# Kernel optimization log

Measured on AMD Instinct MI355X. Metric: run time of the kernel, lower is better.

## Reference

```python
import jax, jax.numpy as jnp
import numpy as np

N, M = 1024, 32
FN, FE = 64, 32
AGG_N, AGG_E = 128, 64
OUT_N, OUT_E = 64, 32


def _build_indices(n, m):
    nip, eip = [], []
    k = 0
    for i in range(1, n):
        j0 = max(0, i - m)
        nip += list(range(j0, i))
        eip += list(range(k, k + i - j0))
        k += i - j0
    n1 = np.array(nip, np.int32)
    eT = np.array(eip, np.int32)
    n2 = np.concatenate([np.full(min(i, m), i, np.int32) for i in range(1, n)])
    # padded previous-node window indices (0 = zero pad slot)
    prev_nodes = np.zeros(n * m, np.int32)
    k = 0
    for i in range(n):
        t = min(i, m)
        prev_nodes[(i + 1) * m - t:(i + 1) * m] = np.arange(k, k + t) + 1
        k += t
    n_e = k
    norm_node = np.full(n, 1.0 / m, np.float32)
    for i in range(1, m):
        norm_node[i] = 1.0 / i
    prev_edges = np.zeros(n_e * m, np.int32)
    k = 0
    e = 0
    for i in range(n):
        j0 = max(0, i - m)
        for j in range(j0, i):
            if j > j0:
                prev_edges[(e + 1) * m - (j - j0):(e + 1) * m] = np.arange(k, k + j - j0) + 1
            e += 1
        k += i - j0
    norm_edge = np.ones(n_e, np.float32)
    k = 0
    for i in range(1, n):
        t = min(i, m)
        for j in range(t):
            if j > 0:
                norm_edge[k] = 1.0 / j
            k += 1
    return n1, eT, n2, prev_nodes, norm_node, prev_edges, norm_edge, n_e

N1, ET, N2, PREV_N, NORM_N, PREV_E, NORM_E, NE = _build_indices(N, M)
N1 = jnp.asarray(N1); ET = jnp.asarray(ET); N2 = jnp.asarray(N2)
PREV_N = jnp.asarray(PREV_N); PREV_E = jnp.asarray(PREV_E)
NORM_N = jnp.asarray(NORM_N); NORM_E = jnp.asarray(NORM_E)


def setup_inputs() -> dict:
    key = jax.random.key(0)
    ks = jax.random.split(key, 20)
    s = 0.02
    inp = {
        'input_nodes': jax.random.normal(ks[0], (2, N, FN), jnp.float32),
        'input_edges': jax.random.normal(ks[1], (2, NE, FE), jnp.float32),
        # node-branch MLPs (exclude_last=False)
        'Wan1': jax.random.normal(ks[2], (2 * FN + FE, 2 * AGG_N)) * s,
        'ban1': jnp.zeros((2 * AGG_N,)),
        'Wan2': jax.random.normal(ks[3], (2 * AGG_N, AGG_N)) * s,
        'ban2': jnp.zeros((AGG_N,)),
        'Wln1': jax.random.normal(ks[4], (AGG_N + FN, AGG_N + FN)) * s,
        'bln1': jnp.zeros((AGG_N + FN,)),
        'Wln2': jax.random.normal(ks[5], (AGG_N + FN, OUT_N)) * s,
        'bln2': jnp.zeros((OUT_N,)),
        # edge-branch MLPs
        'Wae1': jax.random.normal(ks[6], (FN + FE, 2 * AGG_E)) * s,
        'bae1': jnp.zeros((2 * AGG_E,)),
        'Wae2': jax.random.normal(ks[7], (2 * AGG_E, AGG_E)) * s,
        'bae2': jnp.zeros((AGG_E,)),
        'Wle1': jax.random.normal(ks[8], (AGG_E + FE, AGG_E + FE)) * s,
        'ble1': jnp.zeros((AGG_E + FE,)),
        'Wle2': jax.random.normal(ks[9], (AGG_E + FE, OUT_E)) * s,
        'ble2': jnp.zeros((OUT_E,)),
    }
    return inp


def _mlp2(x, W1, b1, W2, b2):
    return jax.nn.relu(jax.nn.relu(x @ W1 + b1) @ W2 + b2)


def reference(input_nodes, input_edges, Wan1, ban1, Wan2, ban2, Wln1, bln1, Wln2, bln2,
              Wae1, bae1, Wae2, bae2, Wle1, ble1, Wle2, ble2):
    B = input_nodes.shape[0]
    # gather node-edge pairs [B, NE, FN+FE] and node-edge-node triples [B, NE, 2FN+FE]
    pairs = jnp.concatenate([input_nodes[:, N1], input_edges[:, ET]], axis=-1)
    triples = jnp.concatenate([input_nodes[:, N1], input_edges[:, ET], input_nodes[:, N2]], axis=-1)
    # node branch (exclude_last=False -> triples)
    hn = _mlp2(triples, Wan1, ban1, Wan2, ban2)                     # [B, NE, AGG_N]
    hn = jnp.concatenate([jnp.zeros((B, 1, AGG_N), hn.dtype), hn], axis=1)
    pn = hn[:, PREV_N].reshape(B, N, M, AGG_N).sum(axis=2)          # padded window sum
    pn = pn * NORM_N[None, :, None]
    nodes_in = jnp.concatenate([pn, input_nodes], axis=-1)
    out_nodes = _mlp2(nodes_in, Wln1, bln1, Wln2, bln2)             # activation_nodes = relu
    # edge branch (pairs)
    he = _mlp2(pairs, Wae1, bae1, Wae2, bae2)                       # [B, NE, AGG_E]
    he = jnp.concatenate([jnp.zeros((B, 1, AGG_E), he.dtype), he], axis=1)
    pe = he[:, PREV_E].reshape(B, NE, M, AGG_E).sum(axis=2)
    pe = pe * NORM_E[None, :, None]
    edges_in = jnp.concatenate([pe, input_edges], axis=-1)
    out_edges = _mlp2(edges_in, Wle1, ble1, Wle2, ble2)             # activation_edges = relu
    return out_nodes, out_edges
```

## Files before the change

### kernel.cpp

```cpp
#include <hip/hip_runtime.h>
#include <cstdint>

#define NN    1024
#define MM    32
#define NEDGE 32240
#define MROWS 64480

typedef unsigned short ushort_t;

typedef __bf16 bf16x8 __attribute__((ext_vector_type(8)));
typedef float  floatx4 __attribute__((ext_vector_type(4)));

__device__ __forceinline__ float b2f(ushort_t u) {
    union { unsigned int i; float f; } v; v.i = ((unsigned int)u) << 16; return v.f;
}
__device__ __forceinline__ ushort_t f2b(float f) {
    unsigned int u = __builtin_bit_cast(unsigned int, f);
    u = (u + 0x7FFFu + ((u >> 16) & 1u)) >> 16;
    return (ushort_t)u;
}
__device__ __forceinline__ int edge_base(int i) {
    return (i <= MM) ? ((i * (i - 1)) >> 1) : (496 + (i - MM) * MM);
}
__device__ __forceinline__ void edge_ij(int e, int& i, int& j) {
    if (e < 496) {
        i = (int)((1.0f + sqrtf(8.0f * (float)e + 1.0f)) * 0.5f);
        while (((i * (i - 1)) >> 1) > e) --i;
        while (((i * (i + 1)) >> 1) <= e) ++i;
        j = e - ((i * (i - 1)) >> 1);
    } else {
        int q = e - 496;
        i = MM + (q >> 5);
        j = i - MM + (q & 31);
    }
}

__global__ __launch_bounds__(256) void k_pack(
        const float* an1, const float* an2, const float* ae1, const float* ae2,
        const float* le1, const float* le2, const float* ln1, const float* ln2,
        const float* nodes, const float* edges,
        ushort_t* pan1, ushort_t* pan2, ushort_t* pae1, ushort_t* pae2,
        ushort_t* ple1, ushort_t* ple2, ushort_t* pln1, ushort_t* pln2,
        ushort_t* nodesb, ushort_t* ein, int2* ijt) {
    __shared__ float tile[32][33];
    const int bid = blockIdx.x;
    const int tid = threadIdx.x;
    if (bid < 152) {
        const float* s; ushort_t* d; int K, N, t;
        if (bid < 40)       { s = an1; d = pan1; K = 160; N = 256; t = bid;       }
        else if (bid < 72)  { s = an2; d = pan2; K = 256; N = 128; t = bid - 40;  }
        else if (bid < 84)  { s = ae1; d = pae1; K = 96;  N = 128; t = bid - 72;  }
        else if (bid < 92)  { s = ae2; d = pae2; K = 128; N = 64;  t = bid - 84;  }
        else if (bid < 101) { s = le1; d = ple1; K = 96;  N = 96;  t = bid - 92;  }
        else if (bid < 104) { s = le2; d = ple2; K = 96;  N = 32;  t = bid - 101; }
        else if (bid < 140) { s = ln1; d = pln1; K = 192; N = 192; t = bid - 104; }
        else                { s = ln2; d = pln2; K = 192; N = 64;  t = bid - 140; }
        int ntn = N >> 5;
        int tk = t / ntn, tn = t - tk * ntn;
        int k0 = tk * 32, n0 = tn * 32;
        int tx = tid & 31, ty = tid >> 5;
#pragma unroll
        for (int m = 0; m < 4; ++m)
            tile[ty + m * 8][tx] = s[(size_t)(k0 + ty + m * 8) * N + n0 + tx];
        __syncthreads();
#pragma unroll
        for (int m = 0; m < 4; ++m)
            d[(size_t)(n0 + ty + m * 8) * K + k0 + tx] = f2b(tile[tx][ty + m * 8]);
    } else if (bid < 280) {
        int i4 = (bid - 152) * 256 + tid;
        float4 v = ((const float4*)nodes)[i4];
        uint2 o;
        o.x = (unsigned)f2b(v.x) | ((unsigned)f2b(v.y) << 16);
        o.y = (unsigned)f2b(v.z) | ((unsigned)f2b(v.w) << 16);
        ((uint2*)nodesb)[i4] = o;
    } else if (bid < 2295) {
        int idx = (bid - 280) * 256 + tid;
        int r = idx >> 3, c4 = idx & 7;
        float4 v = ((const float4*)(edges + (size_t)r * 32))[c4];
        uint2 o;
        o.x = (unsigned)f2b(v.x) | ((unsigned)f2b(v.y) << 16);
        o.y = (unsigned)f2b(v.z) | ((unsigned)f2b(v.w) << 16);
        *(uint2*)(ein + (size_t)r * 96 + 64 + c4 * 4) = o;
    } else {
        int e = (bid - 2295) * 256 + tid;
        if (e < NEDGE) { int i, j; edge_ij(e, i, j); ijt[e] = make_int2(i, j); }
    }
}

__global__ __launch_bounds__(256, 2) void k_agg(
        const ushort_t* __restrict__ nodesb, const float* __restrict__ edges,
        const int2* __restrict__ ijt,
        const ushort_t* __restrict__ pan1, const float* __restrict__ ban1,
        const ushort_t* __restrict__ pan2, const float* __restrict__ ban2,
        const ushort_t* __restrict__ pae1, const float* __restrict__ bae1,
        const ushort_t* __restrict__ pae2, const float* __restrict__ bae2,
        ushort_t* __restrict__ hn, ushort_t* __restrict__ he) {
    __shared__ alignas(16) ushort_t L1[32 * 168];
    __shared__ alignas(16) ushort_t L2[32 * 264];
    const int tid = threadIdx.x;
    const int w = tid >> 6, l = tid & 63, lrow = l & 15, lq = l >> 4;
    floatx4 zero = {0.f, 0.f, 0.f, 0.f};

    if (blockIdx.x < 2015) {
        const int mt = blockIdx.x;
        int2 ij[8];
#pragma unroll
        for (int k = 0; k < 8; ++k) {
            int r = mt * 32 + w * 8 + k;
            int e = (r >= NEDGE) ? r - NEDGE : r;
            ij[k] = ijt[e];
        }
#pragma unroll
        for (int k = 0; k < 8; ++k) {
            int rr = w * 8 + k;
            int r = mt * 32 + rr;
            int b = (r >= NEDGE) ? 1 : 0;
            ushort_t* xr = L1 + rr * 168;
            const unsigned* nj = (const unsigned*)(nodesb + (size_t)(b * NN + ij[k].y) * 64);
            const unsigned* ni = (const unsigned*)(nodesb + (size_t)(b * NN + ij[k].x) * 64);
            if (l < 32) { ((unsigned*)xr)[l] = nj[l]; ((unsigned*)xr)[48 + l] = ni[l]; }
            else        xr[64 + (l - 32)] = f2b(edges[(size_t)r * 32 + (l - 32)]);
        }
        {
            bf16x8 b1[5][4]; float v1[4];
#pragma unroll
            for (int kt = 0; kt < 5; ++kt)
#pragma unroll
                for (int nt = 0; nt < 4; ++nt)
                    b1[kt][nt] = *(const bf16x8*)(pan1 + (size_t)(w * 64 + nt * 16 + lrow) * 160 + kt * 32 + lq * 8);
#pragma unroll
            for (int nt = 0; nt < 4; ++nt) v1[nt] = ban1[w * 64 + nt * 16 + lrow];
            __syncthreads();
            floatx4 acc[2][4];
#pragma unroll
            for (int s = 0; s < 2; ++s)
#pragma unroll
                for (int nt = 0; nt < 4; ++nt) acc[s][nt] = zero;
#pragma unroll
            for (int s = 0; s < 2; ++s)
#pragma unroll
                for (int kt = 0; kt < 5; ++kt) {
                    bf16x8 a = *(const bf16x8*)&L1[(s * 16 + lrow) * 168 + kt * 32 + lq * 8];
#pragma unroll
                    for (int nt = 0; nt < 4; ++nt)
                        acc[s][nt] = __builtin_amdgcn_mfma_f32_16x16x32_bf16(a, b1[kt][nt], acc[s][nt], 0, 0, 0);
                }
#pragma unroll
            for (int s = 0; s < 2; ++s)
#pragma unroll
                for (int nt = 0; nt < 4; ++nt) {
                    int col = w * 64 + nt * 16 + lrow;
#pragma unroll
                    for (int r_ = 0; r_ < 4; ++r_)
                        L2[(s * 16 + lq * 4 + r_) * 264 + col] = f2b(fmaxf(acc[s][nt][r_] + v1[nt], 0.f));
                }
        }
        __syncthreads();
        {
            bf16x8 b2[8][2]; float v2[2];
#pragma unroll
            for (int kt = 0; kt < 8; ++kt)
#pragma unroll
                for (int nt = 0; nt < 2; ++nt)
                    b2[kt][nt] = *(const bf16x8*)(pan2 + (size_t)(w * 32 + nt * 16 + lrow) * 256 + kt * 32 + lq * 8);
#pragma unroll
            for (int nt = 0; nt < 2; ++nt) v2[nt] = ban2[w * 32 + nt * 16 + lrow];
            floatx4 a2[2][2];
#pragma unroll
            for (int s = 0; s < 2; ++s) { a2[s][0] = zero; a2[s][1] = zero; }
#pragma unroll
            for (int s = 0; s < 2; ++s)
#pragma unroll
                for (int kt = 0; kt < 8; ++kt) {
                    bf16x8 a = *(const bf16x8*)&L2[(s * 16 + lrow) * 264 + kt * 32 + lq * 8];
#pragma unroll
                    for (int nt = 0; nt < 2; ++nt)
                        a2[s][nt] = __builtin_amdgcn_mfma_f32_16x16x32_bf16(a, b2[kt][nt], a2[s][nt], 0, 0, 0);
                }
#pragma unroll
            for (int s = 0; s < 2; ++s)
#pragma unroll
                for (int nt = 0; nt < 2; ++nt) {
                    int col = w * 32 + nt * 16 + lrow;
#pragma unroll
                    for (int r_ = 0; r_ < 4; ++r_)
                        hn[(size_t)(mt * 32 + s * 16 + lq * 4 + r_) * 128 + col] = f2b(fmaxf(a2[s][nt][r_] + v2[nt], 0.f));
                }
        }
    } else {
        const int mt = blockIdx.x - 2015;
        int jj[8];
#pragma unroll
        for (int k = 0; k < 8; ++k) {
            int r = mt * 32 + w * 8 + k;
            int e = (r >= NEDGE) ? r - NEDGE : r;
            jj[k] = ijt[e].y;
        }
#pragma unroll
        for (int k = 0; k < 8; ++k) {
            int rr = w * 8 + k;
            int r = mt * 32 + rr;
            int b = (r >= NEDGE) ? 1 : 0;
            ushort_t* xr = L1 + rr * 104;
            const unsigned* nj = (const unsigned*)(nodesb + (size_t)(b * NN + jj[k]) * 64);
            if (l < 32) ((unsigned*)xr)[l] = nj[l];
            else        xr[64 + (l - 32)] = f2b(edges[(size_t)r * 32 + (l - 32)]);
        }
        {
            bf16x8 e1[3][2]; float v1[2];
#pragma unroll
            for (int kt = 0; kt < 3; ++kt)
#pragma unroll
                for (int nt = 0; nt < 2; ++nt)
                    e1[kt][nt] = *(const bf16x8*)(pae1 + (size_t)(w * 32 + nt * 16 + lrow) * 96 + kt * 32 + lq * 8);
#pragma unroll
            for (int nt = 0; nt < 2; ++nt) v1[nt] = bae1[w * 32 + nt * 16 + lrow];
            __syncthreads();
            floatx4 acc[2][2];
#pragma unroll
            for (int s = 0; s < 2; ++s) { acc[s][0] = zero; acc[s][1] = zero; }
#pragma unroll
            for (int s = 0; s < 2; ++s)
#pragma unroll
                for (int kt = 0; kt < 3; ++kt) {
                    bf16x8 a = *(const bf16x8*)&L1[(s * 16 + lrow) * 104 + kt * 32 + lq * 8];
#pragma unroll
                    for (int nt = 0; nt < 2; ++nt)
                        acc[s][nt] = __builtin_amdgcn_mfma_f32_16x16x32_bf16(a, e1[kt][nt], acc[s][nt], 0, 0, 0);
                }
#pragma unroll
            for (int s = 0; s < 2; ++s)
#pragma unroll
                for (int nt = 0; nt < 2; ++nt) {
                    int col = w * 32 + nt * 16 + lrow;
#pragma unroll
                    for (int r_ = 0; r_ < 4; ++r_)
                        L2[(s * 16 + lq * 4 + r_) * 136 + col] = f2b(fmaxf(acc[s][nt][r_] + v1[nt], 0.f));
                }
        }
        __syncthreads();
        {
            bf16x8 e2[4];
#pragma unroll
            for (int kt = 0; kt < 4; ++kt)
                e2[kt] = *(const bf16x8*)(pae2 + (size_t)(w * 16 + lrow) * 128 + kt * 32 + lq * 8);
            float v2 = bae2[w * 16 + lrow];
            floatx4 a2[2] = {zero, zero};
#pragma unroll
            for (int s = 0; s < 2; ++s)
#pragma unroll
                for (int kt = 0; kt < 4; ++kt) {
                    bf16x8 a = *(const bf16x8*)&L2[(s * 16 + lrow) * 136 + kt * 32 + lq * 8];
                    a2[s] = __builtin_amdgcn_mfma_f32_16x16x32_bf16(a, e2[kt], a2[s], 0, 0, 0);
                }
#pragma unroll
            for (int s = 0; s < 2; ++s) {
                int col = w * 16 + lrow;
#pragma unroll
                for (int r_ = 0; r_ < 4; ++r_)
                    he[(size_t)(mt * 32 + s * 16 + lq * 4 + r_) * 64 + col] = f2b(fmaxf(a2[s][r_] + v2, 0.f));
            }
        }
    }
}

__global__ __launch_bounds__(256) void k_mid(
        const ushort_t* __restrict__ hn, const ushort_t* __restrict__ he,
        ushort_t* __restrict__ pn, ushort_t* __restrict__ ein) {
    const int tid = threadIdx.x;
    if (blockIdx.x < 512) {
        int ri = blockIdx.x * 4 + (tid >> 6);
        int l = tid & 63;
        int b = ri >> 10, i = ri & 1023;
        int t = min(i, MM);
        int base = b * NEDGE + edge_base(i);
        const unsigned* hp = (const unsigned*)(hn + (size_t)base * 128) + l;
        float a0 = 0.f, a1 = 0.f, c0 = 0.f, c1 = 0.f;
        int p = 0;
        for (; p + 1 < t; p += 2) {
            unsigned u = hp[(size_t)p * 64];
            unsigned v = hp[(size_t)(p + 1) * 64];
            a0 += b2f((ushort_t)(u & 0xffff)); a1 += b2f((ushort_t)(u >> 16));
            c0 += b2f((ushort_t)(v & 0xffff)); c1 += b2f((ushort_t)(v >> 16));
        }
        if (p < t) {
            unsigned u = hp[(size_t)p * 64];
            a0 += b2f((ushort_t)(u & 0xffff)); a1 += b2f((ushort_t)(u >> 16));
        }
        float inv = 1.0f / (float)max(t, 1);
        unsigned o = (unsigned)f2b((a0 + c0) * inv) | ((unsigned)f2b((a1 + c1) * inv) << 16);
        ((unsigned*)(pn + (size_t)ri * 128))[l] = o;
    } else {
        int bi = blockIdx.x - 512;
        int b = bi >> 10, i = bi & 1023;
        int t = min(i, MM);
        if (t == 0) return;
        int base = b * NEDGE + edge_base(i);
        __shared__ alignas(16) ushort_t hw[32 * 64];
        for (int u = tid; u < t * 8; u += 256)
            ((uint4*)hw)[u] = ((const uint4*)he)[(size_t)base * 8 + u];
        __syncthreads();
        if (tid < 64) {
            float run = 0.f;
            for (int p = 0; p < t; ++p) {
                float v = (p == 0) ? 0.f : run / (float)p;
                ein[(size_t)(base + p) * 96 + tid] = f2b(v);
                run += b2f(hw[p * 64 + tid]);
            }
        }
    }
}

__global__ __launch_bounds__(192) void k_final(
        const ushort_t* __restrict__ pn, const ushort_t* __restrict__ nodesb,
        const ushort_t* __restrict__ pln1, const float* __restrict__ bln1,
        const ushort_t* __restrict__ pln2, const float* __restrict__ bln2,
        float* __restrict__ out_nodes,
        const ushort_t* __restrict__ ein, const ushort_t* __restrict__ ple1,
        const float* __restrict__ ble1, const ushort_t* __restrict__ ple2,
        const float* __restrict__ ble2, float* __restrict__ out_edges) {
    __shared__ alignas(16) ushort_t LA[32 * 200];
    __shared__ alignas(16) ushort_t LB[32 * 200];
    const int tid = threadIdx.x;
    const int w = tid >> 6, l = tid & 63, lrow = l & 15, lq = l >> 4;
    floatx4 zero = {0.f, 0.f, 0.f, 0.f};

    if (blockIdx.x < 64) {
        int tile = blockIdx.x;
        for (int u = tid; u < 768; u += 192) {
            int row = u / 24, c = u - row * 24;
            int ri = tile * 32 + row;
            int b = ri >> 10, i = ri & 1023;
            const uint4* src = (c < 16) ? ((const uint4*)(pn + (size_t)ri * 128) + c)
                                        : ((const uint4*)(nodesb + (size_t)(b * NN + i) * 64) + (c - 16));
            *(uint4*)&LA[row * 200 + c * 8] = *src;
        }
        bf16x8 f1[6][4]; float v1[4];
#pragma unroll
        for (int kt = 0; kt < 6; ++kt)
#pragma unroll
            for (int nt = 0; nt < 4; ++nt)
                f1[kt][nt] = *(const bf16x8*)(pln1 + (size_t)(w * 64 + nt * 16 + lrow) * 192 + kt * 32 + lq * 8);
#pragma unroll
        for (int nt = 0; nt < 4; ++nt) v1[nt] = bln1[w * 64 + nt * 16 + lrow];
        __syncthreads();

        floatx4 acc[2][4];
#pragma unroll
        for (int s = 0; s < 2; ++s)
#pragma unroll
            for (int nt = 0; nt < 4; ++nt) acc[s][nt] = zero;
#pragma unroll
        for (int s = 0; s < 2; ++s)
#pragma unroll
            for (int kt = 0; kt < 6; ++kt) {
                bf16x8 a = *(const bf16x8*)&LA[(s * 16 + lrow) * 200 + kt * 32 + lq * 8];
#pragma unroll
                for (int nt = 0; nt < 4; ++nt)
                    acc[s][nt] = __builtin_amdgcn_mfma_f32_16x16x32_bf16(a, f1[kt][nt], acc[s][nt], 0, 0, 0);
            }
#pragma unroll
        for (int s = 0; s < 2; ++s)
#pragma unroll
            for (int nt = 0; nt < 4; ++nt) {
                int col = w * 64 + nt * 16 + lrow;
#pragma unroll
                for (int r_ = 0; r_ < 4; ++r_)
                    LB[(s * 16 + lq * 4 + r_) * 200 + col] = f2b(fmaxf(acc[s][nt][r_] + v1[nt], 0.f));
            }
        __syncthreads();

        if (w < 2) {
            bf16x8 f2[6][2]; float v2[2];
#pragma unroll
            for (int kt = 0; kt < 6; ++kt)
#pragma unroll
                for (int nt = 0; nt < 2; ++nt)
                    f2[kt][nt] = *(const bf16x8*)(pln2 + (size_t)(w * 32 + nt * 16 + lrow) * 192 + kt * 32 + lq * 8);
#pragma unroll
            for (int nt = 0; nt < 2; ++nt) v2[nt] = bln2[w * 32 + nt * 16 + lrow];
            floatx4 a2[2][2];
#pragma unroll
            for (int s = 0; s < 2; ++s) { a2[s][0] = zero; a2[s][1] = zero; }
#pragma unroll
            for (int s = 0; s < 2; ++s)
#pragma unroll
                for (int kt = 0; kt < 6; ++kt) {
                    bf16x8 a = *(const bf16x8*)&LB[(s * 16 + lrow) * 200 + kt * 32 + lq * 8];
#pragma unroll
                    for (int nt = 0; nt < 2; ++nt)
                        a2[s][nt] = __builtin_amdgcn_mfma_f32_16x16x32_bf16(a, f2[kt][nt], a2[s][nt], 0, 0, 0);
                }
#pragma unroll
            for (int s = 0; s < 2; ++s)
#pragma unroll
                for (int nt = 0; nt < 2; ++nt) {
                    int col = w * 32 + nt * 16 + lrow;
#pragma unroll
                    for (int r_ = 0; r_ < 4; ++r_)
                        out_nodes[(size_t)(tile * 32 + s * 16 + lq * 4 + r_) * 64 + col] =
                            fmaxf(a2[s][nt][r_] + v2[nt], 0.f);
                }
        }
    } else {
        int mt = blockIdx.x - 64;
        for (int k = 0; k < 11; ++k) {
            int rr = w * 11 + k;
            if (rr >= 32) break;
            unsigned* xrow = (unsigned*)(LA + rr * 104);
            const unsigned* src = (const unsigned*)(ein + (size_t)(mt * 32 + rr) * 96);
            if (l < 48) xrow[l] = src[l];
        }
        bf16x8 fb1[3][2]; float v1[2];
#pragma unroll
        for (int kt = 0; kt < 3; ++kt)
#pragma unroll
            for (int nt = 0; nt < 2; ++nt)
                fb1[kt][nt] = *(const bf16x8*)(ple1 + (size_t)(w * 32 + nt * 16 + lrow) * 96 + kt * 32 + lq * 8);
#pragma unroll
        for (int nt = 0; nt < 2; ++nt) v1[nt] = ble1[w * 32 + nt * 16 + lrow];
        bf16x8 fb2[3]; float v2 = 0.f;
        if (w < 2) {
#pragma unroll
            for (int kt = 0; kt < 3; ++kt)
                fb2[kt] = *(const bf16x8*)(ple2 + (size_t)(w * 16 + lrow) * 96 + kt * 32 + lq * 8);
            v2 = ble2[w * 16 + lrow];
        }
        __syncthreads();

        floatx4 acc[2][2];
#pragma unroll
        for (int s = 0; s < 2; ++s) { acc[s][0] = zero; acc[s][1] = zero; }
#pragma unroll
        for (int s = 0; s < 2; ++s)
#pragma unroll
            for (int kt = 0; kt < 3; ++kt) {
                bf16x8 a = *(const bf16x8*)&LA[(s * 16 + lrow) * 104 + kt * 32 + lq * 8];
#pragma unroll
                for (int nt = 0; nt < 2; ++nt)
                    acc[s][nt] = __builtin_amdgcn_mfma_f32_16x16x32_bf16(a, fb1[kt][nt], acc[s][nt], 0, 0, 0);
            }
#pragma unroll
        for (int s = 0; s < 2; ++s)
#pragma unroll
            for (int nt = 0; nt < 2; ++nt) {
                int col = w * 32 + nt * 16 + lrow;
#pragma unroll
                for (int r_ = 0; r_ < 4; ++r_)
                    LB[(s * 16 + lq * 4 + r_) * 104 + col] = f2b(fmaxf(acc[s][nt][r_] + v1[nt], 0.f));
            }
        __syncthreads();

        if (w < 2) {
            floatx4 a2[2] = {zero, zero};
#pragma unroll
            for (int s = 0; s < 2; ++s)
#pragma unroll
                for (int kt = 0; kt < 3; ++kt) {
                    bf16x8 a = *(const bf16x8*)&LB[(s * 16 + lrow) * 104 + kt * 32 + lq * 8];
                    a2[s] = __builtin_amdgcn_mfma_f32_16x16x32_bf16(a, fb2[kt], a2[s], 0, 0, 0);
                }
#pragma unroll
            for (int s = 0; s < 2; ++s) {
                int col = w * 16 + lrow;
#pragma unroll
                for (int r_ = 0; r_ < 4; ++r_)
                    out_edges[(size_t)(mt * 32 + s * 16 + lq * 4 + r_) * 32 + col] = fmaxf(a2[s][r_] + v2, 0.f);
            }
        }
    }
}

extern "C" void kernel_launch(void* const* d_in, const int* in_sizes, int n_in,
                              void* d_out, int out_size, void* d_ws, size_t ws_size,
                              hipStream_t stream) {
    const float* nodes = (const float*)d_in[0];
    const float* edges = (const float*)d_in[1];
    const float* Wan1 = (const float*)d_in[2];  const float* ban1 = (const float*)d_in[3];
    const float* Wan2 = (const float*)d_in[4];  const float* ban2 = (const float*)d_in[5];
    const float* Wln1 = (const float*)d_in[6];  const float* bln1 = (const float*)d_in[7];
    const float* Wln2 = (const float*)d_in[8];  const float* bln2 = (const float*)d_in[9];
    const float* Wae1 = (const float*)d_in[10]; const float* bae1 = (const float*)d_in[11];
    const float* Wae2 = (const float*)d_in[12]; const float* bae2 = (const float*)d_in[13];
    const float* Wle1 = (const float*)d_in[14]; const float* ble1 = (const float*)d_in[15];
    const float* Wle2 = (const float*)d_in[16]; const float* ble2 = (const float*)d_in[17];

    char* ws = (char*)d_ws;
    size_t o = 0;
    auto alloc = [&](size_t bytes) -> void* {
        void* r = ws + o;
        o += (bytes + 255) & ~(size_t)255;
        return r;
    };
    ushort_t* hn     = (ushort_t*)alloc((size_t)MROWS * 128 * 2);
    ushort_t* he     = (ushort_t*)alloc((size_t)MROWS * 64 * 2);
    ushort_t* ein    = (ushort_t*)alloc((size_t)MROWS * 96 * 2);
    ushort_t* pn     = (ushort_t*)alloc((size_t)2048 * 128 * 2);
    ushort_t* nodesb = (ushort_t*)alloc((size_t)2 * NN * 64 * 2);
    int2*     ijt    = (int2*)alloc((size_t)NEDGE * 8);
    ushort_t* pan1 = (ushort_t*)alloc(160 * 256 * 2);
    ushort_t* pan2 = (ushort_t*)alloc(256 * 128 * 2);
    ushort_t* pae1 = (ushort_t*)alloc(96 * 128 * 2);
    ushort_t* pae2 = (ushort_t*)alloc(128 * 64 * 2);
    ushort_t* ple1 = (ushort_t*)alloc(96 * 96 * 2);
    ushort_t* ple2 = (ushort_t*)alloc(96 * 32 * 2);
    ushort_t* pln1 = (ushort_t*)alloc(192 * 192 * 2);
    ushort_t* pln2 = (ushort_t*)alloc(192 * 64 * 2);

    float* out_nodes = (float*)d_out;
    float* out_edges = (float*)d_out + 2 * NN * 64;

    k_pack<<<2421, 256, 0, stream>>>(Wan1, Wan2, Wae1, Wae2, Wle1, Wle2, Wln1, Wln2,
                                     nodes, edges,
                                     pan1, pan2, pae1, pae2, ple1, ple2, pln1, pln2,
                                     nodesb, ein, ijt);
    k_agg<<<4030, 256, 0, stream>>>(nodesb, edges, ijt,
                                    pan1, ban1, pan2, ban2,
                                    pae1, bae1, pae2, bae2, hn, he);
    k_mid<<<2560, 256, 0, stream>>>(hn, he, pn, ein);
    k_final<<<64 + 2015, 192, 0, stream>>>(pn, nodesb, pln1, bln1, pln2, bln2, out_nodes,
                                           ein, ple1, ble1, ple2, ble2, out_edges);

    (void)in_sizes; (void)n_in; (void)out_size; (void)ws_size;
}
```

Baseline: 167.5 us.

## Load MFMA A-operands directly to registers, widen k_agg blocks, split node-window sum

k_agg and k_final now gather each wave's MFMA A fragments straight from global memory into registers instead of staging them in LDS, which removes one LDS round trip and one barrier per tile. k_agg goes from 256 to 512 threads so each wave computes fewer output columns. Its second-layer B-fragment loads are moved before the remaining barrier. In k_mid the node-window sum now uses one block per node, with four wave groups each summing part of the window and a shared-memory reduction at the end. In exchange, every wave reloads the same A rows, so global and L2 traffic rises, and k_agg's higher launch-bounds target tightens the register budget.

```diff
diff --git a/kernel.cpp b/kernel.cpp
--- a/kernel.cpp
+++ b/kernel.cpp
@@ -18,6 +18,12 @@
     unsigned int u = __builtin_bit_cast(unsigned int, f);
     u = (u + 0x7FFFu + ((u >> 16) & 1u)) >> 16;
     return (ushort_t)u;
+}
+__device__ __forceinline__ bf16x8 cvt8(float4 a, float4 b) {
+    union { bf16x8 v; ushort_t u[8]; } r;
+    r.u[0] = f2b(a.x); r.u[1] = f2b(a.y); r.u[2] = f2b(a.z); r.u[3] = f2b(a.w);
+    r.u[4] = f2b(b.x); r.u[5] = f2b(b.y); r.u[6] = f2b(b.z); r.u[7] = f2b(b.w);
+    return r.v;
 }
 __device__ __forceinline__ int edge_base(int i) {
     return (i <= MM) ? ((i * (i - 1)) >> 1) : (496 + (i - MM) * MM);
@@ -87,7 +93,7 @@
     }
 }
 
-__global__ __launch_bounds__(256, 2) void k_agg(
+__global__ __launch_bounds__(512, 4) void k_agg(
         const ushort_t* __restrict__ nodesb, const float* __restrict__ edges,
         const int2* __restrict__ ijt,
         const ushort_t* __restrict__ pan1, const float* __restrict__ ban1,
@@ -95,162 +101,128 @@
         const ushort_t* __restrict__ pae1, const float* __restrict__ bae1,
         const ushort_t* __restrict__ pae2, const float* __restrict__ bae2,
         ushort_t* __restrict__ hn, ushort_t* __restrict__ he) {
-    __shared__ alignas(16) ushort_t L1[32 * 168];
-    __shared__ alignas(16) ushort_t L2[32 * 264];
+    __shared__ alignas(16) ushort_t LS[32 * 264];
     const int tid = threadIdx.x;
     const int w = tid >> 6, l = tid & 63, lrow = l & 15, lq = l >> 4;
     floatx4 zero = {0.f, 0.f, 0.f, 0.f};
 
     if (blockIdx.x < 2015) {
         const int mt = blockIdx.x;
-        int2 ij[8];
-#pragma unroll
-        for (int k = 0; k < 8; ++k) {
-            int r = mt * 32 + w * 8 + k;
-            int e = (r >= NEDGE) ? r - NEDGE : r;
-            ij[k] = ijt[e];
-        }
-#pragma unroll
-        for (int k = 0; k < 8; ++k) {
-            int rr = w * 8 + k;
-            int r = mt * 32 + rr;
-            int b = (r >= NEDGE) ? 1 : 0;
-            ushort_t* xr = L1 + rr * 168;
-            const unsigned* nj = (const unsigned*)(nodesb + (size_t)(b * NN + ij[k].y) * 64);
-            const unsigned* ni = (const unsigned*)(nodesb + (size_t)(b * NN + ij[k].x) * 64);
-            if (l < 32) { ((unsigned*)xr)[l] = nj[l]; ((unsigned*)xr)[48 + l] = ni[l]; }
-            else        xr[64 + (l - 32)] = f2b(edges[(size_t)r * 32 + (l - 32)]);
-        }
-        {
-            bf16x8 b1[5][4]; float v1[4];
+        bf16x8 A[2][5];
+#pragma unroll
+        for (int s = 0; s < 2; ++s) {
+            int r = mt * 32 + s * 16 + lrow;
+            int off = (r >= NEDGE) ? NEDGE : 0;
+            int2 ij = ijt[r - off];
+            int bN = off ? NN : 0;
+            const ushort_t* nj = nodesb + (size_t)(bN + ij.y) * 64;
+            const ushort_t* ni = nodesb + (size_t)(bN + ij.x) * 64;
+            A[s][0] = *(const bf16x8*)(nj + lq * 8);
+            A[s][1] = *(const bf16x8*)(nj + 32 + lq * 8);
+            const float* er = edges + (size_t)r * 32 + lq * 8;
+            A[s][2] = cvt8(*(const float4*)er, *(const float4*)(er + 4));
+            A[s][3] = *(const bf16x8*)(ni + lq * 8);
+            A[s][4] = *(const bf16x8*)(ni + 32 + lq * 8);
+        }
+        bf16x8 b1[5][2]; float v1[2];
+#pragma unroll
+        for (int kt = 0; kt < 5; ++kt)
+#pragma unroll
+            for (int nt = 0; nt < 2; ++nt)
+                b1[kt][nt] = *(const bf16x8*)(pan1 + (size_t)(w * 32 + nt * 16 + lrow) * 160 + kt * 32 + lq * 8);
+#pragma unroll
+        for (int nt = 0; nt < 2; ++nt) v1[nt] = ban1[w * 32 + nt * 16 + lrow];
+
+        floatx4 acc[2][2];
+#pragma unroll
+        for (int s = 0; s < 2; ++s) { acc[s][0] = zero; acc[s][1] = zero; }
+#pragma unroll
+        for (int s = 0; s < 2; ++s)
 #pragma unroll
             for (int kt = 0; kt < 5; ++kt)
 #pragma unroll
-                for (int nt = 0; nt < 4; ++nt)
-                    b1[kt][nt] = *(const bf16x8*)(pan1 + (size_t)(w * 64 + nt * 16 + lrow) * 160 + kt * 32 + lq * 8);
-#pragma unroll
-            for (int nt = 0; nt < 4; ++nt) v1[nt] = ban1[w * 64 + nt * 16 + lrow];
-            __syncthreads();
-            floatx4 acc[2][4];
-#pragma unroll
-            for (int s = 0; s < 2; ++s)
-#pragma unroll
-                for (int nt = 0; nt < 4; ++nt) acc[s][nt] = zero;
-#pragma unroll
-            for (int s = 0; s < 2; ++s)
-#pragma unroll
-                for (int kt = 0; kt < 5; ++kt) {
-                    bf16x8 a = *(const bf16x8*)&L1[(s * 16 + lrow) * 168 + kt * 32 + lq * 8];
-#pragma unroll
-                    for (int nt = 0; nt < 4; ++nt)
-                        acc[s][nt] = __builtin_amdgcn_mfma_f32_16x16x32_bf16(a, b1[kt][nt], acc[s][nt], 0, 0, 0);
-                }
-#pragma unroll
-            for (int s = 0; s < 2; ++s)
-#pragma unroll
-                for (int nt = 0; nt < 4; ++nt) {
-                    int col = w * 64 + nt * 16 + lrow;
-#pragma unroll
-                    for (int r_ = 0; r_ < 4; ++r_)
-                        L2[(s * 16 + lq * 4 + r_) * 264 + col] = f2b(fmaxf(acc[s][nt][r_] + v1[nt], 0.f));
-                }
-        }
-        __syncthreads();
-        {
-            bf16x8 b2[8][2]; float v2[2];
-#pragma unroll
-            for (int kt = 0; kt < 8; ++kt)
-#pragma unroll
                 for (int nt = 0; nt < 2; ++nt)
-                    b2[kt][nt] = *(const bf16x8*)(pan2 + (size_t)(w * 32 + nt * 16 + lrow) * 256 + kt * 32 + lq * 8);
-#pragma unroll
-            for (int nt = 0; nt < 2; ++nt) v2[nt] = ban2[w * 32 + nt * 16 + lrow];
-            floatx4 a2[2][2];
-#pragma unroll
-            for (int s = 0; s < 2; ++s) { a2[s][0] = zero; a2[s][1] = zero; }
-#pragma unroll
-            for (int s = 0; s < 2; ++s)
-#pragma unroll
-                for (int kt = 0; kt < 8; ++kt) {
-                    bf16x8 a = *(const bf16x8*)&L2[(s * 16 + lrow) * 264 + kt * 32 + lq * 8];
-#pragma unroll
-                    for (int nt = 0; nt < 2; ++nt)
-                        a2[s][nt] = __builtin_amdgcn_mfma_f32_16x16x32_bf16(a, b2[kt][nt], a2[s][nt], 0, 0, 0);
-                }
-#pragma unroll
-            for (int s = 0; s < 2; ++s)
-#pragma unroll
-                for (int nt = 0; nt < 2; ++nt) {
-                    int col = w * 32 + nt * 16 + lrow;
-#pragma unroll
-                    for (int r_ = 0; r_ < 4; ++r_)
-                        hn[(size_t)(mt * 32 + s * 16 + lq * 4 + r_) * 128 + col] = f2b(fmaxf(a2[s][nt][r_] + v2[nt], 0.f));
-                }
+                    acc[s][nt] = __builtin_amdgcn_mfma_f32_16x16x32_bf16(A[s][kt], b1[kt][nt], acc[s][nt], 0, 0, 0);
+#pragma unroll
+        for (int s = 0; s < 2; ++s)
+#pragma unroll
+            for (int nt = 0; nt < 2; ++nt) {
+                int col = w * 32 + nt * 16 + lrow;
+#pragma unroll
+                for (int r_ = 0; r_ < 4; ++r_)
+                    LS[(s * 16 + lq * 4 + r_) * 264 + col] = f2b(fmaxf(acc[s][nt][r_] + v1[nt], 0.f));
+            }
+        bf16x8 b2[8];
+#pragma unroll
+        for (int kt = 0; kt < 8; ++kt)
+            b2[kt] = *(const bf16x8*)(pan2 + (size_t)(w * 16 + lrow) * 256 + kt * 32 + lq * 8);
+        float v2 = ban2[w * 16 + lrow];
+        __syncthreads();
+
+        floatx4 a2[2] = {zero, zero};
+#pragma unroll
+        for (int s = 0; s < 2; ++s)
+#pragma unroll
+            for (int kt = 0; kt < 8; ++kt) {
+                bf16x8 a = *(const bf16x8*)&LS[(s * 16 + lrow) * 264 + kt * 32 + lq * 8];
+                a2[s] = __builtin_amdgcn_mfma_f32_16x16x32_bf16(a, b2[kt], a2[s], 0, 0, 0);
+            }
+#pragma unroll
+        for (int s = 0; s < 2; ++s) {
+            int col = w * 16 + lrow;
+#pragma unroll
+            for (int r_ = 0; r_ < 4; ++r_)
+                hn[(size_t)(mt * 32 + s * 16 + lq * 4 + r_) * 128 + col] = f2b(fmaxf(a2[s][r_] + v2, 0.f));
         }
     } else {
         const int mt = blockIdx.x - 2015;
-        int jj[8];
-#pragma unroll
-        for (int k = 0; k < 8; ++k) {
-            int r = mt * 32 + w * 8 + k;
-            int e = (r >= NEDGE) ? r - NEDGE : r;
-            jj[k] = ijt[e].y;
-        }
-#pragma unroll
-        for (int k = 0; k < 8; ++k) {
-            int rr = w * 8 + k;
-            int r = mt * 32 + rr;
-            int b = (r >= NEDGE) ? 1 : 0;
-            ushort_t* xr = L1 + rr * 104;
-            const unsigned* nj = (const unsigned*)(nodesb + (size_t)(b * NN + jj[k]) * 64);
-            if (l < 32) ((unsigned*)xr)[l] = nj[l];
-            else        xr[64 + (l - 32)] = f2b(edges[(size_t)r * 32 + (l - 32)]);
-        }
-        {
-            bf16x8 e1[3][2]; float v1[2];
+        bf16x8 A[2][3];
+#pragma unroll
+        for (int s = 0; s < 2; ++s) {
+            int r = mt * 32 + s * 16 + lrow;
+            int off = (r >= NEDGE) ? NEDGE : 0;
+            int2 ij = ijt[r - off];
+            int bN = off ? NN : 0;
+            const ushort_t* nj = nodesb + (size_t)(bN + ij.y) * 64;
+            A[s][0] = *(const bf16x8*)(nj + lq * 8);
+            A[s][1] = *(const bf16x8*)(nj + 32 + lq * 8);
+            const float* er = edges + (size_t)r * 32 + lq * 8;
+            A[s][2] = cvt8(*(const float4*)er, *(const float4*)(er + 4));
+        }
+        bf16x8 e1[3];
+#pragma unroll
+        for (int kt = 0; kt < 3; ++kt)
+            e1[kt] = *(const bf16x8*)(pae1 + (size_t)(w * 16 + lrow) * 96 + kt * 32 + lq * 8);
+        float v1 = bae1[w * 16 + lrow];
+
+        floatx4 acc[2] = {zero, zero};
+#pragma unroll
+        for (int s = 0; s < 2; ++s)
 #pragma unroll
             for (int kt = 0; kt < 3; ++kt)
-#pragma unroll
-                for (int nt = 0; nt < 2; ++nt)
-                    e1[kt][nt] = *(const bf16x8*)(pae1 + (size_t)(w * 32 + nt * 16 + lrow) * 96 + kt * 32 + lq * 8);
-#pragma unroll
-            for (int nt = 0; nt < 2; ++nt) v1[nt] = bae1[w * 32 + nt * 16 + lrow];
-            __syncthreads();
-            floatx4 acc[2][2];
-#pragma unroll
-            for (int s = 0; s < 2; ++s) { acc[s][0] = zero; acc[s][1] = zero; }
-#pragma unroll
-            for (int s = 0; s < 2; ++s)
-#pragma unroll
-                for (int kt = 0; kt < 3; ++kt) {
-                    bf16x8 a = *(const bf16x8*)&L1[(s * 16 + lrow) * 104 + kt * 32 + lq * 8];
-#pragma unroll
-                    for (int nt = 0; nt < 2; ++nt)
-                        acc[s][nt] = __builtin_amdgcn_mfma_f32_16x16x32_bf16(a, e1[kt][nt], acc[s][nt], 0, 0, 0);
-                }
-#pragma unroll
-            for (int s = 0; s < 2; ++s)
-#pragma unroll
-                for (int nt = 0; nt < 2; ++nt) {
-                    int col = w * 32 + nt * 16 + lrow;
-#pragma unroll
-                    for (int r_ = 0; r_ < 4; ++r_)
-                        L2[(s * 16 + lq * 4 + r_) * 136 + col] = f2b(fmaxf(acc[s][nt][r_] + v1[nt], 0.f));
-                }
-        }
-        __syncthreads();
-        {
-            bf16x8 e2[4];
+                acc[s] = __builtin_amdgcn_mfma_f32_16x16x32_bf16(A[s][kt], e1[kt], acc[s], 0, 0, 0);
+#pragma unroll
+        for (int s = 0; s < 2; ++s) {
+            int col = w * 16 + lrow;
+#pragma unroll
+            for (int r_ = 0; r_ < 4; ++r_)
+                LS[(s * 16 + lq * 4 + r_) * 136 + col] = f2b(fmaxf(acc[s][r_] + v1, 0.f));
+        }
+        bf16x8 e2[4]; float v2 = 0.f;
+        if (w < 4) {
 #pragma unroll
             for (int kt = 0; kt < 4; ++kt)
                 e2[kt] = *(const bf16x8*)(pae2 + (size_t)(w * 16 + lrow) * 128 + kt * 32 + lq * 8);
-            float v2 = bae2[w * 16 + lrow];
+            v2 = bae2[w * 16 + lrow];
+        }
+        __syncthreads();
+        if (w < 4) {
             floatx4 a2[2] = {zero, zero};
 #pragma unroll
             for (int s = 0; s < 2; ++s)
 #pragma unroll
                 for (int kt = 0; kt < 4; ++kt) {
-                    bf16x8 a = *(const bf16x8*)&L2[(s * 16 + lrow) * 136 + kt * 32 + lq * 8];
+                    bf16x8 a = *(const bf16x8*)&LS[(s * 16 + lrow) * 136 + kt * 32 + lq * 8];
                     a2[s] = __builtin_amdgcn_mfma_f32_16x16x32_bf16(a, e2[kt], a2[s], 0, 0, 0);
                 }
 #pragma unroll
@@ -268,30 +240,29 @@
         const ushort_t* __restrict__ hn, const ushort_t* __restrict__ he,
         ushort_t* __restrict__ pn, ushort_t* __restrict__ ein) {
     const int tid = threadIdx.x;
-    if (blockIdx.x < 512) {
-        int ri = blockIdx.x * 4 + (tid >> 6);
-        int l = tid & 63;
+    if (blockIdx.x < 2048) {
+        int ri = blockIdx.x;
         int b = ri >> 10, i = ri & 1023;
         int t = min(i, MM);
         int base = b * NEDGE + edge_base(i);
-        const unsigned* hp = (const unsigned*)(hn + (size_t)base * 128) + l;
-        float a0 = 0.f, a1 = 0.f, c0 = 0.f, c1 = 0.f;
-        int p = 0;
-        for (; p + 1 < t; p += 2) {
-            unsigned u = hp[(size_t)p * 64];
-            unsigned v = hp[(size_t)(p + 1) * 64];
-            a0 += b2f((ushort_t)(u & 0xffff)); a1 += b2f((ushort_t)(u >> 16));
-            c0 += b2f((ushort_t)(v & 0xffff)); c1 += b2f((ushort_t)(v >> 16));
-        }
-        if (p < t) {
-            unsigned u = hp[(size_t)p * 64];
-            a0 += b2f((ushort_t)(u & 0xffff)); a1 += b2f((ushort_t)(u >> 16));
-        }
-        float inv = 1.0f / (float)max(t, 1);
-        unsigned o = (unsigned)f2b((a0 + c0) * inv) | ((unsigned)f2b((a1 + c1) * inv) << 16);
-        ((unsigned*)(pn + (size_t)ri * 128))[l] = o;
+        int c = tid & 63, g = tid >> 6;
+        float s0 = 0.f, s1 = 0.f;
+        for (int p = g; p < t; p += 4) {
+            unsigned u = ((const unsigned*)(hn + (size_t)(base + p) * 128))[c];
+            s0 += b2f((ushort_t)(u & 0xffff));
+            s1 += b2f((ushort_t)(u >> 16));
+        }
+        __shared__ float red[4][128];
+        red[g][c * 2] = s0; red[g][c * 2 + 1] = s1;
+        __syncthreads();
+        if (tid < 64) {
+            float inv = 1.0f / (float)max(t, 1);
+            float a0 = (red[0][tid * 2] + red[1][tid * 2] + red[2][tid * 2] + red[3][tid * 2]) * inv;
+            float a1 = (red[0][tid * 2 + 1] + red[1][tid * 2 + 1] + red[2][tid * 2 + 1] + red[3][tid * 2 + 1]) * inv;
+            ((unsigned*)(pn + (size_t)ri * 128))[tid] = (unsigned)f2b(a0) | ((unsigned)f2b(a1) << 16);
+        }
     } else {
-        int bi = blockIdx.x - 512;
+        int bi = blockIdx.x - 2048;
         int b = bi >> 10, i = bi & 1023;
         int t = min(i, MM);
         if (t == 0) return;
@@ -319,7 +290,6 @@
         const ushort_t* __restrict__ ein, const ushort_t* __restrict__ ple1,
         const float* __restrict__ ble1, const ushort_t* __restrict__ ple2,
         const float* __restrict__ ble2, float* __restrict__ out_edges) {
-    __shared__ alignas(16) ushort_t LA[32 * 200];
     __shared__ alignas(16) ushort_t LB[32 * 200];
     const int tid = threadIdx.x;
     const int w = tid >> 6, l = tid & 63, lrow = l & 15, lq = l >> 4;
@@ -327,13 +297,16 @@
 
     if (blockIdx.x < 64) {
         int tile = blockIdx.x;
-        for (int u = tid; u < 768; u += 192) {
-            int row = u / 24, c = u - row * 24;
-            int ri = tile * 32 + row;
-            int b = ri >> 10, i = ri & 1023;
-            const uint4* src = (c < 16) ? ((const uint4*)(pn + (size_t)ri * 128) + c)
-                                        : ((const uint4*)(nodesb + (size_t)(b * NN + i) * 64) + (c - 16));
-            *(uint4*)&LA[row * 200 + c * 8] = *src;
+        bf16x8 A[2][6];
+#pragma unroll
+        for (int s = 0; s < 2; ++s) {
+            int r = tile * 32 + s * 16 + lrow;
+#pragma unroll
+            for (int kt = 0; kt < 4; ++kt)
+                A[s][kt] = *(const bf16x8*)(pn + (size_t)r * 128 + kt * 32 + lq * 8);
+#pragma unroll
+            for (int kt = 4; kt < 6; ++kt)
+                A[s][kt] = *(const bf16x8*)(nodesb + (size_t)r * 64 + (kt - 4) * 32 + lq * 8);
         }
         bf16x8 f1[6][4]; float v1[4];
 #pragma unroll
@@ -343,7 +316,6 @@
                 f1[kt][nt] = *(const bf16x8*)(pln1 + (size_t)(w * 64 + nt * 16 + lrow) * 192 + kt * 32 + lq * 8);
 #pragma unroll
         for (int nt = 0; nt < 4; ++nt) v1[nt] = bln1[w * 64 + nt * 16 + lrow];
-        __syncthreads();
 
         floatx4 acc[2][4];
 #pragma unroll
@@ -353,12 +325,10 @@
 #pragma unroll
         for (int s = 0; s < 2; ++s)
 #pragma unroll
-            for (int kt = 0; kt < 6; ++kt) {
-                bf16x8 a = *(const bf16x8*)&LA[(s * 16 + lrow) * 200 + kt * 32 + lq * 8];
+            for (int kt = 0; kt < 6; ++kt)
 #pragma unroll
                 for (int nt = 0; nt < 4; ++nt)
-                    acc[s][nt] = __builtin_amdgcn_mfma_f32_16x16x32_bf16(a, f1[kt][nt], acc[s][nt], 0, 0, 0);
-            }
+                    acc[s][nt] = __builtin_amdgcn_mfma_f32_16x16x32_bf16(A[s][kt], f1[kt][nt], acc[s][nt], 0, 0, 0);
 #pragma unroll
         for (int s = 0; s < 2; ++s)
 #pragma unroll
@@ -368,10 +338,8 @@
                 for (int r_ = 0; r_ < 4; ++r_)
                     LB[(s * 16 + lq * 4 + r_) * 200 + col] = f2b(fmaxf(acc[s][nt][r_] + v1[nt], 0.f));
             }
-        __syncthreads();
-
+        bf16x8 f2[6][2]; float v2[2] = {0.f, 0.f};
         if (w < 2) {
-            bf16x8 f2[6][2]; float v2[2];
 #pragma unroll
             for (int kt = 0; kt < 6; ++kt)
 #pragma unroll
@@ -379,6 +347,9 @@
                     f2[kt][nt] = *(const bf16x8*)(pln2 + (size_t)(w * 32 + nt * 16 + lrow) * 192 + kt * 32 + lq * 8);
 #pragma unroll
             for (int nt = 0; nt < 2; ++nt) v2[nt] = bln2[w * 32 + nt * 16 + lrow];
+        }
+        __syncthreads();
+        if (w < 2) {
             floatx4 a2[2][2];
 #pragma unroll
             for (int s = 0; s < 2; ++s) { a2[s][0] = zero; a2[s][1] = zero; }
@@ -404,12 +375,13 @@
         }
     } else {
         int mt = blockIdx.x - 64;
-        for (int k = 0; k < 11; ++k) {
-            int rr = w * 11 + k;
-            if (rr >= 32) break;
-            unsigned* xrow = (unsigned*)(LA + rr * 104);
-            const unsigned* src = (const unsigned*)(ein + (size_t)(mt * 32 + rr) * 96);
-            if (l < 48) xrow[l] = src[l];
+        bf16x8 A[2][3];
+#pragma unroll
+        for (int s = 0; s < 2; ++s) {
+            int r = mt * 32 + s * 16 + lrow;
+#pragma unroll
+            for (int kt = 0; kt < 3; ++kt)
+                A[s][kt] = *(const bf16x8*)(ein + (size_t)r * 96 + kt * 32 + lq * 8);
         }
         bf16x8 fb1[3][2]; float v1[2];
 #pragma unroll
@@ -419,6 +391,26 @@
                 fb1[kt][nt] = *(const bf16x8*)(ple1 + (size_t)(w * 32 + nt * 16 + lrow) * 96 + kt * 32 + lq * 8);
 #pragma unroll
         for (int nt = 0; nt < 2; ++nt) v1[nt] = ble1[w * 32 + nt * 16 + lrow];
+
+        floatx4 acc[2][2];
+#pragma unroll
+        for (int s = 0; s < 2; ++s) { acc[s][0] = zero; acc[s][1] = zero; }
+#pragma unroll
+        for (int s = 0; s < 2; ++s)
+#pragma unroll
+            for (int kt = 0; kt < 3; ++kt)
+#pragma unroll
+                for (int nt = 0; nt < 2; ++nt)
+                    acc[s][nt] = __builtin_amdgcn_mfma_f32_16x16x32_bf16(A[s][kt], fb1[kt][nt], acc[s][nt], 0, 0, 0);
+#pragma unroll
+        for (int s = 0; s < 2; ++s)
+#pragma unroll
+            for (int nt = 0; nt < 2; ++nt) {
+                int col = w * 32 + nt * 16 + lrow;
+#pragma unroll
+                for (int r_ = 0; r_ < 4; ++r_)
+                    LB[(s * 16 + lq * 4 + r_) * 104 + col] = f2b(fmaxf(acc[s][nt][r_] + v1[nt], 0.f));
+            }
         bf16x8 fb2[3]; float v2 = 0.f;
         if (w < 2) {
 #pragma unroll
@@ -427,30 +419,6 @@
             v2 = ble2[w * 16 + lrow];
         }
         __syncthreads();
-
-        floatx4 acc[2][2];
-#pragma unroll
-        for (int s = 0; s < 2; ++s) { acc[s][0] = zero; acc[s][1] = zero; }
-#pragma unroll
-        for (int s = 0; s < 2; ++s)
-#pragma unroll
-            for (int kt = 0; kt < 3; ++kt) {
-                bf16x8 a = *(const bf16x8*)&LA[(s * 16 + lrow) * 104 + kt * 32 + lq * 8];
-#pragma unroll
-                for (int nt = 0; nt < 2; ++nt)
-                    acc[s][nt] = __builtin_amdgcn_mfma_f32_16x16x32_bf16(a, fb1[kt][nt], acc[s][nt], 0, 0, 0);
-            }
-#pragma unroll
-        for (int s = 0; s < 2; ++s)
-#pragma unroll
-            for (int nt = 0; nt < 2; ++nt) {
-                int col = w * 32 + nt * 16 + lrow;
-#pragma unroll
-                for (int r_ = 0; r_ < 4; ++r_)
-                    LB[(s * 16 + lq * 4 + r_) * 104 + col] = f2b(fmaxf(acc[s][nt][r_] + v1[nt], 0.f));
-            }
-        __syncthreads();
-
         if (w < 2) {
             floatx4 a2[2] = {zero, zero};
 #pragma unroll
@@ -514,10 +482,10 @@
                                      nodes, edges,
                                      pan1, pan2, pae1, pae2, ple1, ple2, pln1, pln2,
                                      nodesb, ein, ijt);
-    k_agg<<<4030, 256, 0, stream>>>(nodesb, edges, ijt,
+    k_agg<<<4030, 512, 0, stream>>>(nodesb, edges, ijt,
                                     pan1, ban1, pan2, ban2,
                                     pae1, bae1, pae2, bae2, hn, he);
-    k_mid<<<2560, 256, 0, stream>>>(hn, he, pn, ein);
+    k_mid<<<4096, 256, 0, stream>>>(hn, he, pn, ein);
     k_final<<<64 + 2015, 192, 0, stream>>>(pn, nodesb, pln1, bln1, pln2, bln2, out_nodes,
                                            ein, ple1, ble1, ple2, ble2, out_edges);
 
```

Result: slower. 185.9 us (+11.0%).
